# Optimization experiments

Measured on AMD Instinct MI355X. Metric: run time of the kernel, lower is better.

The kernel has to match this reference:

```python
import jax, jax.numpy as jnp
import numpy as np
from jax import lax

FAN_IN = 16          # fixed number of parents per decoder node
THRESHOLD = 12       # node is active iff >= 12/16 parents are active
K_NODES = 1024       # decoders in this layer
M_PREV = 1024        # nodes in previous layer
N_SPATIAL = 64       # n x n output matrices


def setup_inputs() -> dict:
    key = jax.random.key(0)
    k1, k2, k3, k4, k5 = jax.random.split(key, 5)
    prev_outputs = jax.random.normal(k1, (M_PREV, N_SPATIAL, N_SPATIAL), dtype=jnp.float32)
    # Bernoulli(0.85) so the 12/16 threshold gate is genuinely data-dependent
    prev_is_active = jax.random.bernoulli(k2, 0.85, (M_PREV,))
    parent_indices = jax.random.randint(k3, (K_NODES, FAN_IN), 0, M_PREV, dtype=jnp.int32)
    # Per-node decoder params: 3x3 conv collapsing 16 parent channels -> 1 map, plus bias
    W = jax.random.normal(k4, (K_NODES, FAN_IN, 3, 3), dtype=jnp.float32) * 0.05
    b = jax.random.normal(k5, (K_NODES,), dtype=jnp.float32) * 0.05
    return {"prev_outputs": prev_outputs, "prev_is_active": prev_is_active,
            "parent_indices": parent_indices, "W": W, "b": b}


def reference(prev_outputs, prev_is_active, parent_indices, W, b):
    K, n = parent_indices.shape[0], prev_outputs.shape[-1]
    # Irregular static-wiring gather: (K, 16, n, n) and (K, 16)
    gathered = prev_outputs[parent_indices]
    gathered_flags = prev_is_active[parent_indices]
    # Threshold gate: node active iff >= 12 of its 16 parents are active
    out_active = jnp.sum(gathered_flags.astype(jnp.int32), axis=1) >= THRESHOLD  # (K,)
    # K independent 16->1 convs with distinct weights == one grouped conv (groups = K)
    x = gathered.reshape(1, K * FAN_IN, n, n)          # NCHW
    y = lax.conv_general_dilated(
        x, W, window_strides=(1, 1), padding='SAME',
        dimension_numbers=('NCHW', 'OIHW', 'NCHW'),
        feature_group_count=K,
    )[0]                                               # (K, n, n)
    y = jnp.tanh(y + b[:, None, None])
    # Inactive nodes emit a zero tensor
    out = jnp.where(out_active[:, None, None], y, jnp.zeros((), dtype=y.dtype))
    return out, out_active
```

## Files before the change

kernel.cpp:

```cpp
#include <hip/hip_runtime.h>

#define KN      1024
#define FAN_IN  16
#define NSP     64
#define THRESH  12

__device__ __forceinline__ float tanh_fast(float x) {
    float ax = fabsf(x);
    float e  = __expf(-2.0f * ax);
    float r  = 1.0f - 2.0f * e * __builtin_amdgcn_rcpf(1.0f + e);
    return copysignf(r, x);
}

__device__ __forceinline__ float dpp_wshr1(float x) {
    return __int_as_float(__builtin_amdgcn_update_dpp(
        0, __float_as_int(x), 0x138, 0xF, 0xF, true));
}
__device__ __forceinline__ float dpp_wshl1(float x) {
    return __int_as_float(__builtin_amdgcn_update_dpp(
        0, __float_as_int(x), 0x130, 0xF, 0xF, true));
}

__device__ __forceinline__ void gload_lds16(const float* g, float* l) {
    __builtin_amdgcn_global_load_lds(
        (const __attribute__((address_space(1))) unsigned*)g,
        (__attribute__((address_space(3)))       unsigned*)l,
        16, 0, 0);
}

__global__ __launch_bounds__(512, 8) void decoder_kernel(
    const float* __restrict__ prev_outputs,
    const void*  __restrict__ prev_is_active,
    const int*   __restrict__ parent_indices,
    const float* __restrict__ Wt,
    const float* __restrict__ bias,
    float*       __restrict__ out)
{
    __shared__ float sbuf[2][NSP * NSP];

    const int k    = blockIdx.x;
    const int tid  = threadIdx.x;
    const int lane = tid & 63;
    const int wv   = tid >> 6;
    const int r0   = wv * 8;

    bool bytemode = false;
    {
        const unsigned* sv = (const unsigned*)prev_is_active;
        #pragma unroll
        for (int i = 0; i < 16; ++i)
            if (sv[i] > 1u) bytemode = true;
    }

    const int* pidx = parent_indices + k * FAN_IN;
    int cnt = 0;
    #pragma unroll
    for (int i = 0; i < FAN_IN; ++i) {
        int p = pidx[i];
        int f;
        if (bytemode) f = (((const unsigned char*)prev_is_active)[p] != 0);
        else          f = (((const int*)prev_is_active)[p] != 0);
        cnt += f;
    }
    const bool active = (cnt >= THRESH);

    const size_t obase = (size_t)k * (NSP * NSP);
    if (tid == 0)
        out[(size_t)KN * NSP * NSP + k] = active ? 1.0f : 0.0f;

    if (!active) {
        float4 z = make_float4(0.f, 0.f, 0.f, 0.f);
        float4* o4 = (float4*)(out + obase);
        o4[tid]       = z;
        o4[tid + 512] = z;
        return;
    }

    const float mT = (wv > 0) ? 1.0f : 0.0f;
    const float mB = (wv < 7) ? 1.0f : 0.0f;
    const int   rT = (wv > 0) ? r0 - 1 : 0;
    const int   rB = (wv < 7) ? r0 + 8 : 63;

    const float* wbase = Wt + (size_t)k * FAN_IN * 9;

    float acc[8];
    #pragma unroll
    for (int s = 0; s < 8; ++s) acc[s] = 0.0f;

#define STAGE(buf, p)                                                         \
    {                                                                         \
        const float* g = prev_outputs + (size_t)(p) * (NSP * NSP);            \
        gload_lds16(g + tid * 4,        &sbuf[buf][wv * 256]);                \
        gload_lds16(g + 2048 + tid * 4, &sbuf[buf][2048 + wv * 256]);         \
    }

    STAGE(0, pidx[0]);
    __syncthreads();

    #pragma unroll 2
    for (int ch = 0; ch < FAN_IN; ++ch) {
        if (ch + 1 < FAN_IN) STAGE((ch + 1) & 1, pidx[ch + 1]);

        const float* sb = sbuf[ch & 1];
        const float* w  = wbase + ch * 9;
        const float wl0 = w[0], wc0 = w[1], wr0 = w[2];
        const float wl1 = w[3], wc1 = w[4], wr1 = w[5];
        const float wl2 = w[6], wc2 = w[7], wr2 = w[8];

        float v[10], l[10], r[10];
        v[0] = sb[rT * NSP + lane] * mT;
        #pragma unroll
        for (int j = 1; j <= 8; ++j) v[j] = sb[(r0 - 1 + j) * NSP + lane];
        v[9] = sb[rB * NSP + lane] * mB;
        #pragma unroll
        for (int j = 0; j < 10; ++j) { l[j] = dpp_wshr1(v[j]); r[j] = dpp_wshl1(v[j]); }

        #pragma unroll
        for (int s = 0; s < 8; ++s) {
            float a = acc[s];
            a = fmaf(wl0, l[s],     fmaf(wc0, v[s],     fmaf(wr0, r[s],     a)));
            a = fmaf(wl1, l[s + 1], fmaf(wc1, v[s + 1], fmaf(wr1, r[s + 1], a)));
            a = fmaf(wl2, l[s + 2], fmaf(wc2, v[s + 2], fmaf(wr2, r[s + 2], a)));
            acc[s] = a;
        }

        if (ch + 1 < FAN_IN) __syncthreads();
    }
#undef STAGE

    const float bk = bias[k];
    #pragma unroll
    for (int s = 0; s < 8; ++s)
        out[obase + (size_t)(r0 + s) * NSP + lane] = tanh_fast(acc[s] + bk);
}

extern "C" void kernel_launch(void* const* d_in, const int* in_sizes, int n_in,
                              void* d_out, int out_size, void* d_ws, size_t ws_size,
                              hipStream_t stream) {
    const float* prev_outputs   = (const float*)d_in[0];
    const void*  prev_is_active = d_in[1];
    const int*   parent_indices = (const int*)d_in[2];
    const float* Wt             = (const float*)d_in[3];
    const float* bias           = (const float*)d_in[4];
    float*       out            = (float*)d_out;

    decoder_kernel<<<dim3(KN), dim3(512), 0, stream>>>(
        prev_outputs, prev_is_active, parent_indices, Wt, bias, out);
}
```

Before: 39.10 us.

## Precompress input maps to bf16 and gather half-width maps in decoder

Adds a pre-pass that converts all previous-layer maps to bf16 in the workspace, then the decoder stages bf16 maps into LDS and widens them to fp32 before the stencil. This halves the bytes moved by the irregular 16-parent gather and the LDS footprint. It adds an extra kernel launch plus a full read/write pass over the input, and reduces input precision to bf16, which may affect accuracy tolerance.

```diff
diff --git a/kernel.cpp b/kernel.cpp
--- a/kernel.cpp
+++ b/kernel.cpp
@@ -3,6 +3,7 @@
 #define KN      1024
 #define FAN_IN  16
 #define NSP     64
+#define MAPB    (NSP * NSP)
 #define THRESH  12
 
 __device__ __forceinline__ float tanh_fast(float x) {
@@ -21,14 +22,140 @@
         0, __float_as_int(x), 0x130, 0xF, 0xF, true));
 }
 
-__device__ __forceinline__ void gload_lds16(const float* g, float* l) {
+__device__ __forceinline__ unsigned short f2bf_rne(float x) {
+    unsigned u = __float_as_uint(x);
+    return (unsigned short)((u + 0x7FFFu + ((u >> 16) & 1u)) >> 16);
+}
+__device__ __forceinline__ float bf2f(unsigned short s) {
+    return __uint_as_float(((unsigned)s) << 16);
+}
+
+__global__ __launch_bounds__(256) void compress_kernel(
+    const float* __restrict__ in, unsigned short* __restrict__ out16)
+{
+    const int i = (blockIdx.x * 256 + threadIdx.x) * 4;
+    float4 v = *(const float4*)(in + i);
+    ushort4 o;
+    o.x = f2bf_rne(v.x); o.y = f2bf_rne(v.y);
+    o.z = f2bf_rne(v.z); o.w = f2bf_rne(v.w);
+    *(ushort4*)(out16 + i) = o;
+}
+
+__global__ __launch_bounds__(512, 8) void decoder_bf16(
+    const unsigned short* __restrict__ maps16,
+    const void*  __restrict__ prev_is_active,
+    const int*   __restrict__ parent_indices,
+    const float* __restrict__ Wt,
+    const float* __restrict__ bias,
+    float*       __restrict__ out)
+{
+    __shared__ unsigned short sbuf[2][MAPB];
+
+    const int k    = blockIdx.x;
+    const int tid  = threadIdx.x;
+    const int lane = tid & 63;
+    const int wv   = tid >> 6;
+    const int r0   = wv * 8;
+
+    bool bytemode = false;
+    {
+        const unsigned* sv = (const unsigned*)prev_is_active;
+        #pragma unroll
+        for (int i = 0; i < 16; ++i)
+            if (sv[i] > 1u) bytemode = true;
+    }
+
+    const int* pidx = parent_indices + k * FAN_IN;
+    int cnt = 0;
+    #pragma unroll
+    for (int i = 0; i < FAN_IN; ++i) {
+        int p = pidx[i];
+        int f;
+        if (bytemode) f = (((const unsigned char*)prev_is_active)[p] != 0);
+        else          f = (((const int*)prev_is_active)[p] != 0);
+        cnt += f;
+    }
+    const bool active = (cnt >= THRESH);
+
+    const size_t obase = (size_t)k * MAPB;
+    if (tid == 0)
+        out[(size_t)KN * MAPB + k] = active ? 1.0f : 0.0f;
+
+    if (!active) {
+        float4 z = make_float4(0.f, 0.f, 0.f, 0.f);
+        float4* o4 = (float4*)(out + obase);
+        o4[tid]       = z;
+        o4[tid + 512] = z;
+        return;
+    }
+
+    const float mT = (wv > 0) ? 1.0f : 0.0f;
+    const float mB = (wv < 7) ? 1.0f : 0.0f;
+    const int   rT = (wv > 0) ? r0 - 1 : 0;
+    const int   rB = (wv < 7) ? r0 + 8 : 63;
+
+    const float* wbase = Wt + (size_t)k * FAN_IN * 9;
+
+    float acc[8];
+    #pragma unroll
+    for (int s = 0; s < 8; ++s) acc[s] = 0.0f;
+
+#define STAGE(buf, p)                                                          \
+    __builtin_amdgcn_global_load_lds(                                          \
+        (const __attribute__((address_space(1))) unsigned*)                    \
+            ((const char*)maps16 + (size_t)(p) * 8192 + tid * 16),             \
+        (__attribute__((address_space(3))) unsigned*)                          \
+            ((char*)&sbuf[buf][0] + wv * 1024),                                \
+        16, 0, 0);
+
+    STAGE(0, pidx[0]);
+    __syncthreads();
+
+    #pragma unroll 2
+    for (int ch = 0; ch < FAN_IN; ++ch) {
+        if (ch + 1 < FAN_IN) STAGE((ch + 1) & 1, pidx[ch + 1]);
+
+        const unsigned short* sb = sbuf[ch & 1];
+        const float* w = wbase + ch * 9;
+        const float wl0 = w[0], wc0 = w[1], wr0 = w[2];
+        const float wl1 = w[3], wc1 = w[4], wr1 = w[5];
+        const float wl2 = w[6], wc2 = w[7], wr2 = w[8];
+
+        float v[10], l[10], r[10];
+        v[0] = bf2f(sb[rT * NSP + lane]) * mT;
+        #pragma unroll
+        for (int j = 1; j <= 8; ++j) v[j] = bf2f(sb[(r0 - 1 + j) * NSP + lane]);
+        v[9] = bf2f(sb[rB * NSP + lane]) * mB;
+        #pragma unroll
+        for (int j = 0; j < 10; ++j) { l[j] = dpp_wshr1(v[j]); r[j] = dpp_wshl1(v[j]); }
+
+        #pragma unroll
+        for (int s = 0; s < 8; ++s) {
+            float a = acc[s];
+            a = fmaf(wl0, l[s],     fmaf(wc0, v[s],     fmaf(wr0, r[s],     a)));
+            a = fmaf(wl1, l[s + 1], fmaf(wc1, v[s + 1], fmaf(wr1, r[s + 1], a)));
+            a = fmaf(wl2, l[s + 2], fmaf(wc2, v[s + 2], fmaf(wr2, r[s + 2], a)));
+            acc[s] = a;
+        }
+
+        if (ch + 1 < FAN_IN) __syncthreads();
+    }
+#undef STAGE
+
+    const float bk = bias[k];
+    #pragma unroll
+    for (int s = 0; s < 8; ++s)
+        out[obase + (size_t)(r0 + s) * NSP + lane] = tanh_fast(acc[s] + bk);
+}
+
+__device__ __forceinline__ void gload_lds16f(const float* g, float* l) {
     __builtin_amdgcn_global_load_lds(
         (const __attribute__((address_space(1))) unsigned*)g,
         (__attribute__((address_space(3)))       unsigned*)l,
         16, 0, 0);
 }
 
-__global__ __launch_bounds__(512, 8) void decoder_kernel(
+__global__ __launch_bounds__(512, 8) void decoder_f32(
     const float* __restrict__ prev_outputs,
     const void*  __restrict__ prev_is_active,
     const int*   __restrict__ parent_indices,
@@ -36,7 +163,7 @@
     const float* __restrict__ bias,
     float*       __restrict__ out)
 {
-    __shared__ float sbuf[2][NSP * NSP];
+    __shared__ float sbuf[2][MAPB];
 
     const int k    = blockIdx.x;
     const int tid  = threadIdx.x;
@@ -64,9 +191,9 @@
     }
     const bool active = (cnt >= THRESH);
 
-    const size_t obase = (size_t)k * (NSP * NSP);
+    const size_t obase = (size_t)k * MAPB;
     if (tid == 0)
-        out[(size_t)KN * NSP * NSP + k] = active ? 1.0f : 0.0f;
+        out[(size_t)KN * MAPB + k] = active ? 1.0f : 0.0f;
 
     if (!active) {
         float4 z = make_float4(0.f, 0.f, 0.f, 0.f);
@@ -89,9 +216,9 @@
 
 #define STAGE(buf, p)                                                         \
     {                                                                         \
-        const float* g = prev_outputs + (size_t)(p) * (NSP * NSP);            \
-        gload_lds16(g + tid * 4,        &sbuf[buf][wv * 256]);                \
-        gload_lds16(g + 2048 + tid * 4, &sbuf[buf][2048 + wv * 256]);         \
+        const float* g = prev_outputs + (size_t)(p) * MAPB;                   \
+        gload_lds16f(g + tid * 4,        &sbuf[buf][wv * 256]);               \
+        gload_lds16f(g + 2048 + tid * 4, &sbuf[buf][2048 + wv * 256]);        \
     }
 
     STAGE(0, pidx[0]);
@@ -144,6 +271,15 @@
     const float* bias           = (const float*)d_in[4];
     float*       out            = (float*)d_out;
 
-    decoder_kernel<<<dim3(KN), dim3(512), 0, stream>>>(
-        prev_outputs, prev_is_active, parent_indices, Wt, bias, out);
-}
+    const size_t need = (size_t)KN * MAPB * sizeof(unsigned short);
+    if (ws_size >= need) {
+        unsigned short* maps16 = (unsigned short*)d_ws;
+        compress_kernel<<<dim3(KN * MAPB / (256 * 4)), dim3(256), 0, stream>>>(
+            prev_outputs, maps16);
+        decoder_bf16<<<dim3(KN), dim3(512), 0, stream>>>(
+            maps16, prev_is_active, parent_indices, Wt, bias, out);
+    } else {
+        decoder_f32<<<dim3(KN), dim3(512), 0, stream>>>(
+            prev_outputs, prev_is_active, parent_indices, Wt, bias, out);
+    }
+}
```

Measured after the change: 42.19 us. 7.9% more time.

## Split input channels across wave groups with register loads and LDS reduction

Applied to the files above, without the earlier changes.

The 16 parent channels are now split across four pairs of waves, four channels each. Each wave computes a 32-row half-map by loading its rows straight from global memory into registers, instead of double-buffering every channel through LDS with a block-wide barrier. The four channel-group partial sums are written to an LDS slab and reduced once before bias and tanh. This removes the 15 per-channel __syncthreads and the async LDS staging. In exchange it needs many more registers (32 accumulators plus 34 row values), so the launch-bounds occupancy hint drops from 8 to 4, and it loses the overlap between loading the next channel and computing the current one.

```diff
diff --git a/kernel.cpp b/kernel.cpp
--- a/kernel.cpp
+++ b/kernel.cpp
@@ -3,6 +3,7 @@
 #define KN      1024
 #define FAN_IN  16
 #define NSP     64
+#define MAPB    (NSP * NSP)
 #define THRESH  12
 
 __device__ __forceinline__ float tanh_fast(float x) {
@@ -21,14 +22,7 @@
         0, __float_as_int(x), 0x130, 0xF, 0xF, true));
 }
 
-__device__ __forceinline__ void gload_lds16(const float* g, float* l) {
-    __builtin_amdgcn_global_load_lds(
-        (const __attribute__((address_space(1))) unsigned*)g,
-        (__attribute__((address_space(3)))       unsigned*)l,
-        16, 0, 0);
-}
-
-__global__ __launch_bounds__(512, 8) void decoder_kernel(
+__global__ __launch_bounds__(512, 4) void decoder_kernel(
     const float* __restrict__ prev_outputs,
     const void*  __restrict__ prev_is_active,
     const int*   __restrict__ parent_indices,
@@ -36,13 +30,14 @@
     const float* __restrict__ bias,
     float*       __restrict__ out)
 {
-    __shared__ float sbuf[2][NSP * NSP];
+    __shared__ float slab[8][32][NSP];
 
     const int k    = blockIdx.x;
     const int tid  = threadIdx.x;
     const int lane = tid & 63;
     const int wv   = tid >> 6;
-    const int r0   = wv * 8;
+    const int g    = wv >> 1;
+    const int h    = wv & 1;
 
     bool bytemode = false;
     {
@@ -64,9 +59,9 @@
     }
     const bool active = (cnt >= THRESH);
 
-    const size_t obase = (size_t)k * (NSP * NSP);
+    const size_t obase = (size_t)k * MAPB;
     if (tid == 0)
-        out[(size_t)KN * NSP * NSP + k] = active ? 1.0f : 0.0f;
+        out[(size_t)KN * MAPB + k] = active ? 1.0f : 0.0f;
 
     if (!active) {
         float4 z = make_float4(0.f, 0.f, 0.f, 0.f);
@@ -76,62 +71,67 @@
         return;
     }
 
-    const float mT = (wv > 0) ? 1.0f : 0.0f;
-    const float mB = (wv < 7) ? 1.0f : 0.0f;
-    const int   rT = (wv > 0) ? r0 - 1 : 0;
-    const int   rB = (wv < 7) ? r0 + 8 : 63;
+    const int   gbase = h * 32 - 1;
+    const float mT = (h == 1) ? 1.0f : 0.0f;
+    const float mB = (h == 0) ? 1.0f : 0.0f;
+    const int   gT = (h == 1) ? 31 : 0;
+    const int   gB = (h == 0) ? 32 : 63;
 
     const float* wbase = Wt + (size_t)k * FAN_IN * 9;
 
-    float acc[8];
+    float acc[32];
     #pragma unroll
-    for (int s = 0; s < 8; ++s) acc[s] = 0.0f;
+    for (int a = 0; a < 32; ++a) acc[a] = 0.0f;
 
-#define STAGE(buf, p)                                                         \
-    {                                                                         \
-        const float* g = prev_outputs + (size_t)(p) * (NSP * NSP);            \
-        gload_lds16(g + tid * 4,        &sbuf[buf][wv * 256]);                \
-        gload_lds16(g + 2048 + tid * 4, &sbuf[buf][2048 + wv * 256]);         \
+    #pragma unroll 1
+    for (int cc = 0; cc < 4; ++cc) {
+        const int ch = g * 4 + cc;
+        const int p  = pidx[ch];
+        const float* __restrict__ src = prev_outputs + (size_t)p * MAPB + lane;
+
+        float row[34];
+        row[0] = src[gT * NSP] * mT;
+        #pragma unroll
+        for (int j = 1; j <= 32; ++j) row[j] = src[(gbase + j) * NSP];
+        row[33] = src[gB * NSP] * mB;
+
+        const float* w = wbase + ch * 9;
+        const float wl[3] = { w[0], w[3], w[6] };
+        const float wc[3] = { w[1], w[4], w[7] };
+        const float wr[3] = { w[2], w[5], w[8] };
+
+        #pragma unroll
+        for (int j = 0; j < 34; ++j) {
+            const float l = dpp_wshr1(row[j]);
+            const float r = dpp_wshl1(row[j]);
+            #pragma unroll
+            for (int t = 0; t < 3; ++t) {
+                const int a = j - t;
+                if (a >= 0 && a < 32)
+                    acc[a] = fmaf(wl[t], l,
+                              fmaf(wc[t], row[j],
+                               fmaf(wr[t], r, acc[a])));
+            }
+        }
     }
 
-    STAGE(0, pidx[0]);
+    #pragma unroll
+    for (int a = 0; a < 32; ++a) slab[wv][a][lane] = acc[a];
+
     __syncthreads();
-
-    #pragma unroll 2
-    for (int ch = 0; ch < FAN_IN; ++ch) {
-        if (ch + 1 < FAN_IN) STAGE((ch + 1) & 1, pidx[ch + 1]);
-
-        const float* sb = sbuf[ch & 1];
-        const float* w  = wbase + ch * 9;
-        const float wl0 = w[0], wc0 = w[1], wr0 = w[2];
-        const float wl1 = w[3], wc1 = w[4], wr1 = w[5];
-        const float wl2 = w[6], wc2 = w[7], wr2 = w[8];
-
-        float v[10], l[10], r[10];
-        v[0] = sb[rT * NSP + lane] * mT;
-        #pragma unroll
-        for (int j = 1; j <= 8; ++j) v[j] = sb[(r0 - 1 + j) * NSP + lane];
-        v[9] = sb[rB * NSP + lane] * mB;
-        #pragma unroll
-        for (int j = 0; j < 10; ++j) { l[j] = dpp_wshr1(v[j]); r[j] = dpp_wshl1(v[j]); }
-
-        #pragma unroll
-        for (int s = 0; s < 8; ++s) {
-            float a = acc[s];
-            a = fmaf(wl0, l[s],     fmaf(wc0, v[s],     fmaf(wr0, r[s],     a)));
-            a = fmaf(wl1, l[s + 1], fmaf(wc1, v[s + 1], fmaf(wr1, r[s + 1], a)));
-            a = fmaf(wl2, l[s + 2], fmaf(wc2, v[s + 2], fmaf(wr2, r[s + 2], a)));
-            acc[s] = a;
-        }
-
-        if (ch + 1 < FAN_IN) __syncthreads();
-    }
-#undef STAGE
 
     const float bk = bias[k];
     #pragma unroll
-    for (int s = 0; s < 8; ++s)
-        out[obase + (size_t)(r0 + s) * NSP + lane] = tanh_fast(acc[s] + bk);
+    for (int n = 0; n < 8; ++n) {
+        const int i   = tid + n * 512;
+        const int r_  = i >> 6;
+        const int col = i & 63;
+        const int h2  = r_ >> 5;
+        const int a   = r_ & 31;
+        const float s = slab[h2][a][col] + slab[2 + h2][a][col]
+                      + slab[4 + h2][a][col] + slab[6 + h2][a][col];
+        out[obase + (size_t)r_ * NSP + col] = tanh_fast(s + bk);
+    }
 }
 
 extern "C" void kernel_launch(void* const* d_in, const int* in_sizes, int n_in,
```

After: 49.74 us. +27.2%, slower.

## Triple-buffer parent map staging with explicit vmcnt waits and single barrier

Applied to the files above, without the earlier changes.

Moves the LDS staging of parent maps from double to triple buffering, so two channels are in flight ahead of compute. Each iteration now uses a single barrier, waiting with s_waitcnt vmcnt(2) only for the oldest outstanding stage instead of a full __syncthreads. The goal is to hide more gather latency from global memory and cut synchronisation overhead. The trade-off is 48KB of LDS per block instead of 32KB, and the min-blocks launch bound is dropped, which can lower occupancy on a kernel that is already close to bandwidth-bound.

```diff
diff --git a/kernel.cpp b/kernel.cpp
--- a/kernel.cpp
+++ b/kernel.cpp
@@ -3,6 +3,7 @@
 #define KN      1024
 #define FAN_IN  16
 #define NSP     64
+#define MAPB    (NSP * NSP)
 #define THRESH  12
 
 __device__ __forceinline__ float tanh_fast(float x) {
@@ -21,14 +22,14 @@
         0, __float_as_int(x), 0x130, 0xF, 0xF, true));
 }
 
-__device__ __forceinline__ void gload_lds16(const float* g, float* l) {
+__device__ __forceinline__ void gload_lds16f(const float* g, float* l) {
     __builtin_amdgcn_global_load_lds(
         (const __attribute__((address_space(1))) unsigned*)g,
         (__attribute__((address_space(3)))       unsigned*)l,
         16, 0, 0);
 }
 
-__global__ __launch_bounds__(512, 8) void decoder_kernel(
+__global__ __launch_bounds__(512) void decoder_kernel(
     const float* __restrict__ prev_outputs,
     const void*  __restrict__ prev_is_active,
     const int*   __restrict__ parent_indices,
@@ -36,7 +37,7 @@
     const float* __restrict__ bias,
     float*       __restrict__ out)
 {
-    __shared__ float sbuf[2][NSP * NSP];
+    __shared__ float sbuf[3][MAPB];
 
     const int k    = blockIdx.x;
     const int tid  = threadIdx.x;
@@ -64,9 +65,9 @@
     }
     const bool active = (cnt >= THRESH);
 
-    const size_t obase = (size_t)k * (NSP * NSP);
+    const size_t obase = (size_t)k * MAPB;
     if (tid == 0)
-        out[(size_t)KN * NSP * NSP + k] = active ? 1.0f : 0.0f;
+        out[(size_t)KN * MAPB + k] = active ? 1.0f : 0.0f;
 
     if (!active) {
         float4 z = make_float4(0.f, 0.f, 0.f, 0.f);
@@ -87,46 +88,58 @@
     #pragma unroll
     for (int s = 0; s < 8; ++s) acc[s] = 0.0f;
 
-#define STAGE(buf, p)                                                         \
+#define STAGE(b, ch)                                                          \
     {                                                                         \
-        const float* g = prev_outputs + (size_t)(p) * (NSP * NSP);            \
-        gload_lds16(g + tid * 4,        &sbuf[buf][wv * 256]);                \
-        gload_lds16(g + 2048 + tid * 4, &sbuf[buf][2048 + wv * 256]);         \
+        const float* g = prev_outputs + (size_t)pidx[ch] * MAPB;              \
+        gload_lds16f(g + tid * 4,        &sbuf[b][wv * 256]);                 \
+        gload_lds16f(g + 2048 + tid * 4, &sbuf[b][2048 + wv * 256]);          \
     }
 
-    STAGE(0, pidx[0]);
-    __syncthreads();
+#define COMPUTE(sb_, ch)                                                      \
+    {                                                                         \
+        const float* sb = (sb_);                                              \
+        const float* w  = wbase + (ch) * 9;                                   \
+        const float wl0 = w[0], wc0 = w[1], wr0 = w[2];                       \
+        const float wl1 = w[3], wc1 = w[4], wr1 = w[5];                       \
+        const float wl2 = w[6], wc2 = w[7], wr2 = w[8];                       \
+        float v[10], l[10], r[10];                                            \
+        v[0] = sb[rT * NSP + lane] * mT;                                      \
+        _Pragma("unroll")                                                     \
+        for (int j = 1; j <= 8; ++j) v[j] = sb[(r0 - 1 + j) * NSP + lane];    \
+        v[9] = sb[rB * NSP + lane] * mB;                                      \
+        _Pragma("unroll")                                                     \
+        for (int j = 0; j < 10; ++j) { l[j] = dpp_wshr1(v[j]); r[j] = dpp_wshl1(v[j]); } \
+        _Pragma("unroll")                                                     \
+        for (int s = 0; s < 8; ++s) {                                         \
+            float a = acc[s];                                                 \
+            a = fmaf(wl0, l[s],     fmaf(wc0, v[s],     fmaf(wr0, r[s],     a))); \
+            a = fmaf(wl1, l[s + 1], fmaf(wc1, v[s + 1], fmaf(wr1, r[s + 1], a))); \
+            a = fmaf(wl2, l[s + 2], fmaf(wc2, v[s + 2], fmaf(wr2, r[s + 2], a))); \
+            acc[s] = a;                                                       \
+        }                                                                     \
+    }
 
-    #pragma unroll 2
-    for (int ch = 0; ch < FAN_IN; ++ch) {
-        if (ch + 1 < FAN_IN) STAGE((ch + 1) & 1, pidx[ch + 1]);
+    STAGE(0, 0);
+    STAGE(1, 1);
 
-        const float* sb = sbuf[ch & 1];
-        const float* w  = wbase + ch * 9;
-        const float wl0 = w[0], wc0 = w[1], wr0 = w[2];
-        const float wl1 = w[3], wc1 = w[4], wr1 = w[5];
-        const float wl2 = w[6], wc2 = w[7], wr2 = w[8];
+    #pragma unroll 1
+    for (int ch = 0; ch < FAN_IN - 1; ++ch) {
+        asm volatile("s_waitcnt vmcnt(2)" ::: "memory");
+        __builtin_amdgcn_s_barrier();
+        __builtin_amdgcn_sched_barrier(0);
 
-        float v[10], l[10], r[10];
-        v[0] = sb[rT * NSP + lane] * mT;
-        #pragma unroll
-        for (int j = 1; j <= 8; ++j) v[j] = sb[(r0 - 1 + j) * NSP + lane];
-        v[9] = sb[rB * NSP + lane] * mB;
-        #pragma unroll
-        for (int j = 0; j < 10; ++j) { l[j] = dpp_wshr1(v[j]); r[j] = dpp_wshl1(v[j]); }
+        COMPUTE(sbuf[ch % 3], ch);
 
-        #pragma unroll
-        for (int s = 0; s < 8; ++s) {
-            float a = acc[s];
-            a = fmaf(wl0, l[s],     fmaf(wc0, v[s],     fmaf(wr0, r[s],     a)));
-            a = fmaf(wl1, l[s + 1], fmaf(wc1, v[s + 1], fmaf(wr1, r[s + 1], a)));
-            a = fmaf(wl2, l[s + 2], fmaf(wc2, v[s + 2], fmaf(wr2, r[s + 2], a)));
-            acc[s] = a;
-        }
+        if (ch + 2 < FAN_IN) STAGE((ch + 2) % 3, ch + 2);
+    }
 
-        if (ch + 1 < FAN_IN) __syncthreads();
-    }
+    asm volatile("s_waitcnt vmcnt(0)" ::: "memory");
+    __builtin_amdgcn_s_barrier();
+    __builtin_amdgcn_sched_barrier(0);
+    COMPUTE(sbuf[(FAN_IN - 1) % 3], FAN_IN - 1);
+
 #undef STAGE
+#undef COMPUTE
 
     const float bk = bias[k];
     #pragma unroll
```

Result: slower. 41.88 us (+7.1%).
